# Optimization experiments

Hardware: AMD Instinct MI355X
Metric: run time of the kernel (lower is better)

## Reference

```python
import jax, jax.numpy as jnp
import numpy as np


def _fps(xyz, npoint):
    # Farthest point sampling, vectorized over batch, lax.scan over iterations.
    # Deterministic start at index 0 (torch uses a random start index).
    B, N, _ = xyz.shape
    binds = jnp.arange(B)

    def step(carry, _):
        dist_min, far = carry
        centroid = xyz[binds, far][:, None, :]              # [B,1,3]
        d = jnp.sum((xyz - centroid) ** 2, axis=-1)         # [B,N]
        dist_min = jnp.minimum(dist_min, d)
        return (dist_min, jnp.argmax(dist_min, axis=-1)), far

    init = (jnp.full((B, N), 1e10, xyz.dtype), jnp.zeros((B,), jnp.int32))
    _, cents = jax.lax.scan(step, init, None, length=npoint)
    return cents.T                                           # [B,npoint]


def setup_inputs() -> dict:
    key = jax.random.key(0)
    ks = jax.random.split(key, 8)
    B, N, Cp = 16, 4096, 64
    return {
        "xyz": jax.random.normal(ks[0], (B, N, 3), jnp.float32),
        "points": jax.random.normal(ks[1], (B, Cp, N), jnp.float32),
        "W1": jax.random.normal(ks[2], (64, 67), jnp.float32) * 0.1,
        "b1": jnp.zeros((64,), jnp.float32),
        "W2": jax.random.normal(ks[3], (64, 64), jnp.float32) * 0.1,
        "b2": jnp.zeros((64,), jnp.float32),
        "W3": jax.random.normal(ks[4], (128, 64), jnp.float32) * 0.1,
        "b3": jnp.zeros((128,), jnp.float32),
        "npoint": 1024,
        "k": 32,
    }


def reference(xyz, points, W1, b1, W2, b2, W3, b3, npoint, k):
    B, N, _ = xyz.shape
    binds = jnp.arange(B)

    # FPS -> centroid coords
    cent_idx = _fps(xyz, npoint)                              # [B,S]
    new_xyz = jnp.take_along_axis(xyz, cent_idx[..., None], axis=1)  # [B,S,3]

    # KNN via squared distances (same argsort order as euclidean cdist)
    d2 = (jnp.sum(new_xyz ** 2, -1)[..., None]
          + jnp.sum(xyz ** 2, -1)[:, None, :]
          - 2.0 * jnp.einsum('bsc,bnc->bsn', new_xyz, xyz))   # [B,S,N]
    _, idx = jax.lax.top_k(-d2, k)                            # [B,S,K]

    # Gather-grouping (channels-last; equivalent math to channel-first conv1x1)
    grouped_xyz = xyz[binds[:, None, None], idx]              # [B,S,K,3]
    grouped_pts = points.transpose(0, 2, 1)[binds[:, None, None], idx]  # [B,S,K,Cp]
    grouped = jnp.concatenate([grouped_xyz, grouped_pts], axis=-1)      # [B,S,K,67]

    # Conv2d(k=1) stack == per-point MLP
    h = jax.nn.relu(jnp.einsum('bskc,oc->bsko', grouped, W1) + b1)
    h = jax.nn.relu(jnp.einsum('bskc,oc->bsko', h, W2) + b2)
    h = jax.nn.relu(jnp.einsum('bskc,oc->bsko', h, W3) + b3)  # [B,S,K,128]

    new_points = jnp.max(h, axis=2).transpose(0, 2, 1)        # [B,128,S]
    return new_xyz, new_points
```

## Files before the change

kernel.cpp:

```cpp
#include <hip/hip_runtime.h>
#include <hip/hip_bf16.h>
#include <stdint.h>
#include <string.h>

#define BB   16
#define NN   4096
#define NP   1024
#define KK   32
#define CP   64
#define CIN  67
#define H3   128

typedef __attribute__((ext_vector_type(8))) short short8;
typedef __attribute__((ext_vector_type(4))) float floatx4;
typedef __attribute__((ext_vector_type(2))) float f32x2;

__device__ __forceinline__ float sq3_exact(float x, float y, float z) {
#pragma clang fp contract(off)
    float a = x * x;
    float b = y * y;
    float c = z * z;
    return (a + b) + c;
}
__device__ __forceinline__ float dot3_exact(float ax, float ay, float az,
                                            float bx, float by, float bz) {
#pragma clang fp contract(off)
    float a = ax * bx;
    float b = ay * by;
    float c = az * bz;
    return (a + b) + c;
}
__device__ __forceinline__ float d2_exact(float sn, float sx, float dt) {
#pragma clang fp contract(off)
    return (sn + sx) - 2.0f * dt;
}
__device__ __forceinline__ uint32_t f32_sortable(float f) {
    uint32_t u = __float_as_uint(f);
    return u ^ ((uint32_t)((int32_t)u >> 31) | 0x80000000u);
}
__device__ __forceinline__ unsigned long long umax64(unsigned long long a, unsigned long long b) {
    return a > b ? a : b;
}
__device__ __forceinline__ uint32_t umax32(uint32_t a, uint32_t b) { return a > b ? a : b; }
__device__ __forceinline__ unsigned short bf16_bits(float f) {
    __hip_bfloat16 h = __float2bfloat16(f);
    unsigned short us;
    __builtin_memcpy(&us, &h, 2);
    return us;
}

template <int CTRL>
__device__ __forceinline__ uint32_t dpp_umax32_step(uint32_t k) {
    uint32_t o = (uint32_t)__builtin_amdgcn_update_dpp(0, (int)k, CTRL, 0xf, 0xf, true);
    return k > o ? k : o;
}
__device__ __forceinline__ uint32_t wave_umax32_dpp(uint32_t k) {
    k = dpp_umax32_step<0x111>(k);
    k = dpp_umax32_step<0x112>(k);
    k = dpp_umax32_step<0x114>(k);
    k = dpp_umax32_step<0x118>(k);
    k = dpp_umax32_step<0x142>(k);
    k = dpp_umax32_step<0x143>(k);
    return (uint32_t)__builtin_amdgcn_readlane((int)k, 63);
}

__global__ void __launch_bounds__(256) transpose_pts(const float* __restrict__ pts,
                                                     __hip_bfloat16* __restrict__ ptsT) {
    __shared__ float tile[64][65];
    int b  = blockIdx.y;
    int n0 = blockIdx.x * 64;
    int tx = threadIdx.x & 63, ty = threadIdx.x >> 6;
    const float* src = pts + (size_t)b * CP * NN;
    for (int c = ty; c < 64; c += 4)
        tile[c][tx] = src[c * NN + n0 + tx];
    __syncthreads();
    __hip_bfloat16* dst = ptsT + ((size_t)b * NN + n0) * CP;
    for (int nn2 = ty; nn2 < 64; nn2 += 4)
        dst[nn2 * CP + tx] = __float2bfloat16(tile[tx][nn2]);
}

__global__ void __launch_bounds__(256) prep_weights(const float* __restrict__ W1,
                                                    const float* __restrict__ W2,
                                                    const float* __restrict__ W3,
                                                    short* __restrict__ w1p,
                                                    short* __restrict__ w2p,
                                                    short* __restrict__ w3p) {
    int tid = blockIdx.x * 256 + threadIdx.x;
    int tot = gridDim.x * 256;
    for (int i = tid; i < 64 * 96; i += tot) {
        int o = i / 96, c = i % 96;
        float v = (c < 64) ? W1[o * CIN + 3 + c] : ((c < 67) ? W1[o * CIN + (c - 64)] : 0.0f);
        w1p[i] = (short)bf16_bits(v);
    }
    for (int i = tid; i < 64 * 64; i += tot)  w2p[i] = (short)bf16_bits(W2[i]);
    for (int i = tid; i < 128 * 64; i += tot) w3p[i] = (short)bf16_bits(W3[i]);
}

#define FPS_T 256

__global__ void __launch_bounds__(FPS_T, 1) fps_kernel(const float* __restrict__ xyz,
                                                       float* __restrict__ newxyz) {
    __shared__ __attribute__((aligned(16))) float4 sxyz[NN];
    __shared__ int farr[NP];
    __shared__ __attribute__((aligned(16))) unsigned long long kbuf[2][4];
    int b = blockIdx.x;
    int tid = threadIdx.x;
    const float* xb = xyz + (size_t)b * NN * 3;
    f32x2 px2[8], py2[8], pz2[8], dm2[8];
#pragma unroll
    for (int jj = 0; jj < 8; jj++) {
        int n0 = jj * 512 + tid;
        int n1 = n0 + 256;
        float x0 = xb[n0 * 3 + 0], y0 = xb[n0 * 3 + 1], z0 = xb[n0 * 3 + 2];
        float x1 = xb[n1 * 3 + 0], y1 = xb[n1 * 3 + 1], z1 = xb[n1 * 3 + 2];
        px2[jj] = (f32x2){x0, x1}; py2[jj] = (f32x2){y0, y1}; pz2[jj] = (f32x2){z0, z1};
        sxyz[n0] = make_float4(x0, y0, z0, 0.0f);
        sxyz[n1] = make_float4(x1, y1, z1, 0.0f);
        dm2[jj] = (f32x2){1e10f, 1e10f};
    }
#pragma unroll
    for (int jj = 0; jj < 8; jj++) {
        asm volatile("" : "+v"(px2[jj]), "+v"(py2[jj]), "+v"(pz2[jj]));
    }
    if (tid == 0) farr[0] = 0;
    __syncthreads();
    int far = 0;
    for (int t = 0; t < NP - 1; t++) {
        float4 c = sxyz[far];
        f32x2 ccx = (f32x2){c.x, c.x};
        f32x2 ccy = (f32x2){c.y, c.y};
        f32x2 ccz = (f32x2){c.z, c.z};
        float bv = -1.0f; int bn = 0;
#pragma unroll
        for (int jj = 0; jj < 8; jj++) {
            f32x2 dx, dy, dz, xx, yy, zz, s01, s;
            asm("v_pk_add_f32 %0, %1, %2 neg_lo:[0,1] neg_hi:[0,1]" : "=v"(dx) : "v"(px2[jj]), "v"(ccx));
            asm("v_pk_add_f32 %0, %1, %2 neg_lo:[0,1] neg_hi:[0,1]" : "=v"(dy) : "v"(py2[jj]), "v"(ccy));
            asm("v_pk_add_f32 %0, %1, %2 neg_lo:[0,1] neg_hi:[0,1]" : "=v"(dz) : "v"(pz2[jj]), "v"(ccz));
            asm("v_pk_mul_f32 %0, %1, %1" : "=v"(xx) : "v"(dx));
            asm("v_pk_mul_f32 %0, %1, %1" : "=v"(yy) : "v"(dy));
            asm("v_pk_mul_f32 %0, %1, %1" : "=v"(zz) : "v"(dz));
            asm("v_pk_add_f32 %0, %1, %2" : "=v"(s01) : "v"(xx), "v"(yy));
            asm("v_pk_add_f32 %0, %1, %2" : "=v"(s)   : "v"(s01), "v"(zz));
            float d0 = fminf(dm2[jj].x, s.x);
            dm2[jj].x = d0;
            bn = (d0 > bv) ? (jj * 512 + tid) : bn;
            bv = fmaxf(bv, d0);
            float d1 = fminf(dm2[jj].y, s.y);
            dm2[jj].y = d1;
            bn = (d1 > bv) ? (jj * 512 + 256 + tid) : bn;
            bv = fmaxf(bv, d1);
        }
        uint32_t bvb = __float_as_uint(bv);
        uint32_t m = wave_umax32_dpp(bvb);
        unsigned long long mask = __ballot(bvb == m);
        int n_sel;
        if (__popcll(mask) == 1) {
            n_sel = __builtin_amdgcn_readlane(bn, (int)(__ffsll((unsigned long long)mask) - 1));
        } else {
            uint32_t cand = (bvb == m) ? (uint32_t)bn : 0xFFFFFFFFu;
            n_sel = (int)~wave_umax32_dpp(~cand);
        }
        int par = t & 1;
        if ((tid & 63) == 0)
            kbuf[par][tid >> 6] = ((unsigned long long)m << 32) | (unsigned)(NN - 1 - n_sel);
        __syncthreads();
        const ulonglong2* kp = (const ulonglong2*)kbuf[par];
        ulonglong2 k0 = kp[0], k1 = kp[1];
        unsigned long long mm = umax64(umax64(k0.x, k0.y), umax64(k1.x, k1.y));
        far = NN - 1 - (int)(unsigned)(mm & 0xFFFFFFFFull);
        if (tid == 0) farr[t + 1] = far;
    }
    __syncthreads();
    float* nxb = newxyz + (size_t)b * NP * 3;
    for (int t = tid; t < NP; t += FPS_T) {
        float4 p = sxyz[farr[t]];
        nxb[t * 3 + 0] = p.x;
        nxb[t * 3 + 1] = p.y;
        nxb[t * 3 + 2] = p.z;
    }
}

__global__ void __launch_bounds__(64) knn_kernel(const float* __restrict__ xyz,
                                                 const float* __restrict__ newxyz,
                                                 unsigned short* __restrict__ knn_out) {
    __shared__ uint32_t keys[64 * 64];
    int s = blockIdx.x, b = blockIdx.y, lane = threadIdx.x;
    const float* c3 = newxyz + ((size_t)b * NP + s) * 3;
    float cx = c3[0], cy = c3[1], cz = c3[2];
    float sn = sq3_exact(cx, cy, cz);
    const float* xb = xyz + (size_t)b * NN * 3;
    uint32_t gv[8];
#pragma unroll
    for (int g = 0; g < 8; g++) gv[g] = 0;
#pragma unroll
    for (int j = 0; j < 64; j++) {
        int n = j * 64 + lane;
        float x = xb[n * 3 + 0], y = xb[n * 3 + 1], z = xb[n * 3 + 2];
        float sx = sq3_exact(x, y, z);
        float dt = dot3_exact(cx, cy, cz, x, y, z);
        float d2 = d2_exact(sn, sx, dt);
        uint32_t ck = ~f32_sortable(d2);
        keys[j * 64 + lane] = ck;
        gv[j >> 3] = umax32(gv[j >> 3], ck);
    }
    uint32_t best = 0;
#pragma unroll
    for (int g = 0; g < 8; g++) best = umax32(best, gv[g]);

    unsigned short* out = knn_out + ((size_t)b * NP + s) * KK;
    for (int r = 0; r < KK; r++) {
        uint32_t m = wave_umax32_dpp(best);
        unsigned long long mask = __ballot(best == m);
        bool cand = (best == m);
        uint32_t myn = 0xFFFFFFFFu;
        int gsel = 7, jl = 7;
        uint32_t grp[8];
        if (cand) {
#pragma unroll
            for (int g = 6; g >= 0; g--) if (gv[g] == m) gsel = g;
#pragma unroll
            for (int q = 0; q < 8; q++) grp[q] = keys[(gsel * 8 + q) * 64 + lane];
#pragma unroll
            for (int q = 6; q >= 0; q--) if (grp[q] == m) jl = q;
            myn = (uint32_t)((gsel * 8 + jl) * 64 + lane);
        }
        uint32_t n_sel;
        if (__popcll(mask) > 1) {
            n_sel = ~wave_umax32_dpp(~myn);
        } else {
            n_sel = (uint32_t)__builtin_amdgcn_readlane((int)myn,
                        (int)(__ffsll((unsigned long long)mask) - 1));
        }
        if (lane == 0) out[r] = (unsigned short)n_sel;
        if (cand && myn == n_sel) {
            keys[(gsel * 8 + jl) * 64 + lane] = 0;
#pragma unroll
            for (int q = 0; q < 8; q++) grp[q] = (q == jl) ? 0u : grp[q];
            uint32_t nv = 0;
#pragma unroll
            for (int q = 0; q < 8; q++) nv = umax32(nv, grp[q]);
#pragma unroll
            for (int g = 0; g < 8; g++) gv[g] = (g == gsel) ? nv : gv[g];
            best = 0;
#pragma unroll
            for (int g = 0; g < 8; g++) best = umax32(best, gv[g]);
        }
    }
}

#define MLP_WSZ (32 * 96 + 32 * 72)

__global__ void __launch_bounds__(256) mlp_mfma(const float* __restrict__ xyz,
                                                const __hip_bfloat16* __restrict__ ptsT,
                                                const unsigned short* __restrict__ knni,
                                                const short* __restrict__ w1p,
                                                const short* __restrict__ w2p,
                                                const short* __restrict__ w3p,
                                                const float* __restrict__ b1,
                                                const float* __restrict__ b2,
                                                const float* __restrict__ b3,
                                                float* __restrict__ out_np) {
    __shared__ __attribute__((aligned(16))) short lds[4 * MLP_WSZ];
    int tid  = threadIdx.x;
    int wave = tid >> 6, lane = tid & 63;
    int l15  = lane & 15, quad = lane >> 4;
    int gid  = blockIdx.x * 4 + wave;
    int b    = gid >> 10, s = gid & (NP - 1);
    short* Gw  = lds + wave * MLP_WSZ;
    short* h1w = Gw + 32 * 96;
    short* h2w = Gw;

    float b1v[4], b2v[4], b3v[8];
#pragma unroll
    for (int i = 0; i < 4; i++) b1v[i] = b1[l15 + 16 * i];
#pragma unroll
    for (int i = 0; i < 4; i++) b2v[i] = b2[l15 + 16 * i];
#pragma unroll
    for (int i = 0; i < 8; i++) b3v[i] = b3[l15 + 16 * i];

    {
        int r = lane & 31, h = lane >> 5;
        int n = (int)knni[(size_t)gid * KK + r];
        const short8* prow = (const short8*)(ptsT + ((size_t)b * NN + n) * CP);
        short8 c0 = prow[h * 4 + 0], c1 = prow[h * 4 + 1];
        short8 c2 = prow[h * 4 + 2], c3 = prow[h * 4 + 3];
        short8* gdst = (short8*)&Gw[r * 96];
        gdst[h * 4 + 0] = c0; gdst[h * 4 + 1] = c1;
        gdst[h * 4 + 2] = c2; gdst[h * 4 + 3] = c3;
        short8 z8 = {0, 0, 0, 0, 0, 0, 0, 0};
        if (h == 0) {
            const float* xp = xyz + ((size_t)b * NN + n) * 3;
            short8 v = z8;
            v[0] = (short)bf16_bits(xp[0]);
            v[1] = (short)bf16_bits(xp[1]);
            v[2] = (short)bf16_bits(xp[2]);
            gdst[8] = v; gdst[9] = z8;
        } else {
            gdst[10] = z8; gdst[11] = z8;
        }
    }

    {
        floatx4 acc[2][4];
#pragma unroll
        for (int mt = 0; mt < 2; mt++)
#pragma unroll
            for (int nt = 0; nt < 4; nt++) acc[mt][nt] = (floatx4)0.0f;
#pragma unroll
        for (int kt = 0; kt < 3; kt++) {
            short8 a0 = *(const short8*)&Gw[(l15) * 96 + kt * 32 + quad * 8];
            short8 a1 = *(const short8*)&Gw[(l15 + 16) * 96 + kt * 32 + quad * 8];
#pragma unroll
            for (int nt = 0; nt < 4; nt++) {
                short8 bf = *(const short8*)&w1p[(l15 + 16 * nt) * 96 + kt * 32 + quad * 8];
                acc[0][nt] = __builtin_amdgcn_mfma_f32_16x16x32_bf16(a0, bf, acc[0][nt], 0, 0, 0);
                acc[1][nt] = __builtin_amdgcn_mfma_f32_16x16x32_bf16(a1, bf, acc[1][nt], 0, 0, 0);
            }
        }
#pragma unroll
        for (int mt = 0; mt < 2; mt++)
#pragma unroll
            for (int nt = 0; nt < 4; nt++)
#pragma unroll
                for (int r = 0; r < 4; r++) {
                    float v = fmaxf(acc[mt][nt][r] + b1v[nt], 0.0f);
                    h1w[(quad * 4 + r + 16 * mt) * 72 + l15 + 16 * nt] = (short)bf16_bits(v);
                }
    }

    {
        floatx4 acc[2][4];
#pragma unroll
        for (int mt = 0; mt < 2; mt++)
#pragma unroll
            for (int nt = 0; nt < 4; nt++) acc[mt][nt] = (floatx4)0.0f;
#pragma unroll
        for (int kt = 0; kt < 2; kt++) {
            short8 a0 = *(const short8*)&h1w[(l15) * 72 + kt * 32 + quad * 8];
            short8 a1 = *(const short8*)&h1w[(l15 + 16) * 72 + kt * 32 + quad * 8];
#pragma unroll
            for (int nt = 0; nt < 4; nt++) {
                short8 bf = *(const short8*)&w2p[(l15 + 16 * nt) * 64 + kt * 32 + quad * 8];
                acc[0][nt] = __builtin_amdgcn_mfma_f32_16x16x32_bf16(a0, bf, acc[0][nt], 0, 0, 0);
                acc[1][nt] = __builtin_amdgcn_mfma_f32_16x16x32_bf16(a1, bf, acc[1][nt], 0, 0, 0);
            }
        }
#pragma unroll
        for (int mt = 0; mt < 2; mt++)
#pragma unroll
            for (int nt = 0; nt < 4; nt++)
#pragma unroll
                for (int r = 0; r < 4; r++) {
                    float v = fmaxf(acc[mt][nt][r] + b2v[nt], 0.0f);
                    h2w[(quad * 4 + r + 16 * mt) * 72 + l15 + 16 * nt] = (short)bf16_bits(v);
                }
    }

    {
        floatx4 acc[2][8];
#pragma unroll
        for (int mt = 0; mt < 2; mt++)
#pragma unroll
            for (int nt = 0; nt < 8; nt++) acc[mt][nt] = (floatx4)0.0f;
#pragma unroll
        for (int kt = 0; kt < 2; kt++) {
            short8 a0 = *(const short8*)&h2w[(l15) * 72 + kt * 32 + quad * 8];
            short8 a1 = *(const short8*)&h2w[(l15 + 16) * 72 + kt * 32 + quad * 8];
#pragma unroll
            for (int nt = 0; nt < 8; nt++) {
                short8 bf = *(const short8*)&w3p[(l15 + 16 * nt) * 64 + kt * 32 + quad * 8];
                acc[0][nt] = __builtin_amdgcn_mfma_f32_16x16x32_bf16(a0, bf, acc[0][nt], 0, 0, 0);
                acc[1][nt] = __builtin_amdgcn_mfma_f32_16x16x32_bf16(a1, bf, acc[1][nt], 0, 0, 0);
            }
        }
#pragma unroll
        for (int nt = 0; nt < 8; nt++) {
            float m = acc[0][nt][0];
#pragma unroll
            for (int r = 1; r < 4; r++) m = fmaxf(m, acc[0][nt][r]);
#pragma unroll
            for (int r = 0; r < 4; r++) m = fmaxf(m, acc[1][nt][r]);
            m = fmaxf(m, __shfl_xor(m, 16));
            m = fmaxf(m, __shfl_xor(m, 32));
            m = fmaxf(m + b3v[nt], 0.0f);
            if (lane < 16)
                out_np[((size_t)b * H3 + l15 + 16 * nt) * NP + s] = m;
        }
    }
}

extern "C" void kernel_launch(void* const* d_in, const int* in_sizes, int n_in,
                              void* d_out, int out_size, void* d_ws, size_t ws_size,
                              hipStream_t stream) {
    (void)in_sizes; (void)n_in; (void)out_size; (void)ws_size;
    const float* xyz = (const float*)d_in[0];
    const float* pts = (const float*)d_in[1];
    const float* W1  = (const float*)d_in[2];
    const float* b1  = (const float*)d_in[3];
    const float* W2  = (const float*)d_in[4];
    const float* b2  = (const float*)d_in[5];
    const float* W3  = (const float*)d_in[6];
    const float* b3  = (const float*)d_in[7];

    float* out    = (float*)d_out;
    float* newxyz = out;
    float* newpts = out + (size_t)BB * NP * 3;

    char* ws = (char*)d_ws;
    __hip_bfloat16* ptsT = (__hip_bfloat16*)ws;
    unsigned short* knni = (unsigned short*)(ws + (size_t)BB * NN * CP * 2);
    short* w1p = (short*)(ws + 9437184);
    short* w2p = w1p + 64 * 96;
    short* w3p = w2p + 64 * 64;

    transpose_pts<<<dim3(NN / 64, BB), 256, 0, stream>>>(pts, ptsT);
    prep_weights <<<64, 256, 0, stream>>>(W1, W2, W3, w1p, w2p, w3p);
    fps_kernel   <<<BB, FPS_T, 0, stream>>>(xyz, newxyz);
    knn_kernel   <<<dim3(NP, BB), 64, 0, stream>>>(xyz, newxyz, knni);
    mlp_mfma     <<<dim3(BB * NP / 4), 256, 0, stream>>>(xyz, ptsT, knni,
                                                         w1p, w2p, w3p, b1, b2, b3, newpts);
}
```

Measured before the change: 907.0 us.

## Fuse FPS, KNN and MLP into one persistent kernel with centroid publishing

Replaces the separate FPS, KNN and MLP launches with a single persistent kernel. The first 16 blocks run FPS at raised priority and publish each centroid index to global memory with atomic stores. The remaining worker waves spin on those flags and run KNN plus the MLP per centroid, interleaved across batches. This overlaps the serial FPS latency with the KNN/MLP work and removes the KNN index round-trip through global memory. The cost is spin-wait polling, and correctness depends on the FPS blocks being co-resident with the workers so the spinning cannot deadlock.

Result: faster. 762.2 us (-16.0%).

```diff
diff --git a/kernel.cpp b/kernel.cpp
--- a/kernel.cpp
+++ b/kernel.cpp
@@ -10,6 +10,11 @@
 #define CP   64
 #define CIN  67
 #define H3   128
+
+#define FPS_T   256
+#define NWORKB  496
+#define NGRID   (BB + NWORKB)
+#define NWAVES  (NWORKB * 4)
 
 typedef __attribute__((ext_vector_type(8))) short short8;
 typedef __attribute__((ext_vector_type(4))) float floatx4;
@@ -84,9 +89,11 @@
                                                     const float* __restrict__ W3,
                                                     short* __restrict__ w1p,
                                                     short* __restrict__ w2p,
-                                                    short* __restrict__ w3p) {
+                                                    short* __restrict__ w3p,
+                                                    uint32_t* __restrict__ centpub) {
     int tid = blockIdx.x * 256 + threadIdx.x;
     int tot = gridDim.x * 256;
+    for (int i = tid; i < BB * NP; i += tot) centpub[i] = 0u;
     for (int i = tid; i < 64 * 96; i += tot) {
         int o = i / 96, c = i % 96;
         float v = (c < 64) ? W1[o * CIN + 3 + c] : ((c < 67) ? W1[o * CIN + (c - 64)] : 0.0f);
@@ -96,180 +103,118 @@
     for (int i = tid; i < 128 * 64; i += tot) w3p[i] = (short)bf16_bits(W3[i]);
 }
 
-#define FPS_T 256
-
-__global__ void __launch_bounds__(FPS_T, 1) fps_kernel(const float* __restrict__ xyz,
-                                                       float* __restrict__ newxyz) {
-    __shared__ __attribute__((aligned(16))) float4 sxyz[NN];
-    __shared__ int farr[NP];
-    __shared__ __attribute__((aligned(16))) unsigned long long kbuf[2][4];
-    int b = blockIdx.x;
+__global__ void __launch_bounds__(256, 2)
+fused_kernel(const float* __restrict__ xyz,
+             const __hip_bfloat16* __restrict__ ptsT,
+             const short* __restrict__ w1p,
+             const short* __restrict__ w2p,
+             const short* __restrict__ w3p,
+             const float* __restrict__ b1,
+             const float* __restrict__ b2,
+             const float* __restrict__ b3,
+             uint32_t* __restrict__ centpub,
+             float* __restrict__ out) {
+    __shared__ __attribute__((aligned(16))) char smem[69696];
     int tid = threadIdx.x;
-    const float* xb = xyz + (size_t)b * NN * 3;
-    f32x2 px2[8], py2[8], pz2[8], dm2[8];
-#pragma unroll
-    for (int jj = 0; jj < 8; jj++) {
-        int n0 = jj * 512 + tid;
-        int n1 = n0 + 256;
-        float x0 = xb[n0 * 3 + 0], y0 = xb[n0 * 3 + 1], z0 = xb[n0 * 3 + 2];
-        float x1 = xb[n1 * 3 + 0], y1 = xb[n1 * 3 + 1], z1 = xb[n1 * 3 + 2];
-        px2[jj] = (f32x2){x0, x1}; py2[jj] = (f32x2){y0, y1}; pz2[jj] = (f32x2){z0, z1};
-        sxyz[n0] = make_float4(x0, y0, z0, 0.0f);
-        sxyz[n1] = make_float4(x1, y1, z1, 0.0f);
-        dm2[jj] = (f32x2){1e10f, 1e10f};
+
+    if (blockIdx.x < BB) {
+        asm volatile("s_setprio 3");
+        float4* sxyz = (float4*)smem;
+        int*    farr = (int*)(smem + 65536);
+        unsigned long long* kbufp = (unsigned long long*)(smem + 69632);
+        int b = blockIdx.x;
+        uint32_t* pub = centpub + b * NP;
+        const float* xb = xyz + (size_t)b * NN * 3;
+        if (tid == 0)
+            __hip_atomic_store(&pub[0], 0x10000u, __ATOMIC_RELAXED, __HIP_MEMORY_SCOPE_AGENT);
+        f32x2 px2[8], py2[8], pz2[8], dm2[8];
+#pragma unroll
+        for (int jj = 0; jj < 8; jj++) {
+            int n0 = jj * 512 + tid;
+            int n1 = n0 + 256;
+            float x0 = xb[n0 * 3 + 0], y0 = xb[n0 * 3 + 1], z0 = xb[n0 * 3 + 2];
+            float x1 = xb[n1 * 3 + 0], y1 = xb[n1 * 3 + 1], z1 = xb[n1 * 3 + 2];
+            px2[jj] = (f32x2){x0, x1}; py2[jj] = (f32x2){y0, y1}; pz2[jj] = (f32x2){z0, z1};
+            sxyz[n0] = make_float4(x0, y0, z0, 0.0f);
+            sxyz[n1] = make_float4(x1, y1, z1, 0.0f);
+            dm2[jj] = (f32x2){1e10f, 1e10f};
+        }
+#pragma unroll
+        for (int jj = 0; jj < 8; jj++) {
+            asm volatile("" : "+v"(px2[jj]), "+v"(py2[jj]), "+v"(pz2[jj]));
+        }
+        if (tid == 0) farr[0] = 0;
+        __syncthreads();
+        int far = 0;
+        for (int t = 0; t < NP - 1; t++) {
+            float4 c = sxyz[far];
+            f32x2 ccx = (f32x2){c.x, c.x};
+            f32x2 ccy = (f32x2){c.y, c.y};
+            f32x2 ccz = (f32x2){c.z, c.z};
+            float bv = -1.0f; int bn = 0;
+#pragma unroll
+            for (int jj = 0; jj < 8; jj++) {
+                f32x2 dx, dy, dz, xx, yy, zz, s01, s;
+                asm("v_pk_add_f32 %0, %1, %2 neg_lo:[0,1] neg_hi:[0,1]" : "=v"(dx) : "v"(px2[jj]), "v"(ccx));
+                asm("v_pk_add_f32 %0, %1, %2 neg_lo:[0,1] neg_hi:[0,1]" : "=v"(dy) : "v"(py2[jj]), "v"(ccy));
+                asm("v_pk_add_f32 %0, %1, %2 neg_lo:[0,1] neg_hi:[0,1]" : "=v"(dz) : "v"(pz2[jj]), "v"(ccz));
+                asm("v_pk_mul_f32 %0, %1, %1" : "=v"(xx) : "v"(dx));
+                asm("v_pk_mul_f32 %0, %1, %1" : "=v"(yy) : "v"(dy));
+                asm("v_pk_mul_f32 %0, %1, %1" : "=v"(zz) : "v"(dz));
+                asm("v_pk_add_f32 %0, %1, %2" : "=v"(s01) : "v"(xx), "v"(yy));
+                asm("v_pk_add_f32 %0, %1, %2" : "=v"(s)   : "v"(s01), "v"(zz));
+                float d0 = fminf(dm2[jj].x, s.x);
+                dm2[jj].x = d0;
+                bn = (d0 > bv) ? (jj * 512 + tid) : bn;
+                bv = fmaxf(bv, d0);
+                float d1 = fminf(dm2[jj].y, s.y);
+                dm2[jj].y = d1;
+                bn = (d1 > bv) ? (jj * 512 + 256 + tid) : bn;
+                bv = fmaxf(bv, d1);
+            }
+            uint32_t bvb = __float_as_uint(bv);
+            uint32_t m = wave_umax32_dpp(bvb);
+            unsigned long long mask = __ballot(bvb == m);
+            int n_sel;
+            if (__popcll(mask) == 1) {
+                n_sel = __builtin_amdgcn_readlane(bn, (int)(__ffsll((unsigned long long)mask) - 1));
+            } else {
+                uint32_t cand = (bvb == m) ? (uint32_t)bn : 0xFFFFFFFFu;
+                n_sel = (int)~wave_umax32_dpp(~cand);
+            }
+            int par = t & 1;
+            if ((tid & 63) == 0)
+                kbufp[par * 4 + (tid >> 6)] =
+                    ((unsigned long long)m << 32) | (unsigned)(NN - 1 - n_sel);
+            __syncthreads();
+            const ulonglong2* kp = (const ulonglong2*)(kbufp + par * 4);
+            ulonglong2 k0 = kp[0], k1 = kp[1];
+            unsigned long long mm = umax64(umax64(k0.x, k0.y), umax64(k1.x, k1.y));
+            far = NN - 1 - (int)(unsigned)(mm & 0xFFFFFFFFull);
+            if (tid == 0) {
+                farr[t + 1] = far;
+                __hip_atomic_store(&pub[t + 1], 0x10000u | (uint32_t)far,
+                                   __ATOMIC_RELAXED, __HIP_MEMORY_SCOPE_AGENT);
+            }
+        }
+        __syncthreads();
+        float* nxb = out + (size_t)b * NP * 3;
+        for (int t = tid; t < NP; t += FPS_T) {
+            float4 p = sxyz[farr[t]];
+            nxb[t * 3 + 0] = p.x;
+            nxb[t * 3 + 1] = p.y;
+            nxb[t * 3 + 2] = p.z;
+        }
+        return;
     }
-#pragma unroll
-    for (int jj = 0; jj < 8; jj++) {
-        asm volatile("" : "+v"(px2[jj]), "+v"(py2[jj]), "+v"(pz2[jj]));
-    }
-    if (tid == 0) farr[0] = 0;
-    __syncthreads();
-    int far = 0;
-    for (int t = 0; t < NP - 1; t++) {
-        float4 c = sxyz[far];
-        f32x2 ccx = (f32x2){c.x, c.x};
-        f32x2 ccy = (f32x2){c.y, c.y};
-        f32x2 ccz = (f32x2){c.z, c.z};
-        float bv = -1.0f; int bn = 0;
-#pragma unroll
-        for (int jj = 0; jj < 8; jj++) {
-            f32x2 dx, dy, dz, xx, yy, zz, s01, s;
-            asm("v_pk_add_f32 %0, %1, %2 neg_lo:[0,1] neg_hi:[0,1]" : "=v"(dx) : "v"(px2[jj]), "v"(ccx));
-            asm("v_pk_add_f32 %0, %1, %2 neg_lo:[0,1] neg_hi:[0,1]" : "=v"(dy) : "v"(py2[jj]), "v"(ccy));
-            asm("v_pk_add_f32 %0, %1, %2 neg_lo:[0,1] neg_hi:[0,1]" : "=v"(dz) : "v"(pz2[jj]), "v"(ccz));
-            asm("v_pk_mul_f32 %0, %1, %1" : "=v"(xx) : "v"(dx));
-            asm("v_pk_mul_f32 %0, %1, %1" : "=v"(yy) : "v"(dy));
-            asm("v_pk_mul_f32 %0, %1, %1" : "=v"(zz) : "v"(dz));
-            asm("v_pk_add_f32 %0, %1, %2" : "=v"(s01) : "v"(xx), "v"(yy));
-            asm("v_pk_add_f32 %0, %1, %2" : "=v"(s)   : "v"(s01), "v"(zz));
-            float d0 = fminf(dm2[jj].x, s.x);
-            dm2[jj].x = d0;
-            bn = (d0 > bv) ? (jj * 512 + tid) : bn;
-            bv = fmaxf(bv, d0);
-            float d1 = fminf(dm2[jj].y, s.y);
-            dm2[jj].y = d1;
-            bn = (d1 > bv) ? (jj * 512 + 256 + tid) : bn;
-            bv = fmaxf(bv, d1);
-        }
-        uint32_t bvb = __float_as_uint(bv);
-        uint32_t m = wave_umax32_dpp(bvb);
-        unsigned long long mask = __ballot(bvb == m);
-        int n_sel;
-        if (__popcll(mask) == 1) {
-            n_sel = __builtin_amdgcn_readlane(bn, (int)(__ffsll((unsigned long long)mask) - 1));
-        } else {
-            uint32_t cand = (bvb == m) ? (uint32_t)bn : 0xFFFFFFFFu;
-            n_sel = (int)~wave_umax32_dpp(~cand);
-        }
-        int par = t & 1;
-        if ((tid & 63) == 0)
-            kbuf[par][tid >> 6] = ((unsigned long long)m << 32) | (unsigned)(NN - 1 - n_sel);
-        __syncthreads();
-        const ulonglong2* kp = (const ulonglong2*)kbuf[par];
-        ulonglong2 k0 = kp[0], k1 = kp[1];
-        unsigned long long mm = umax64(umax64(k0.x, k0.y), umax64(k1.x, k1.y));
-        far = NN - 1 - (int)(unsigned)(mm & 0xFFFFFFFFull);
-        if (tid == 0) farr[t + 1] = far;
-    }
-    __syncthreads();
-    float* nxb = newxyz + (size_t)b * NP * 3;
-    for (int t = tid; t < NP; t += FPS_T) {
-        float4 p = sxyz[farr[t]];
-        nxb[t * 3 + 0] = p.x;
-        nxb[t * 3 + 1] = p.y;
-        nxb[t * 3 + 2] = p.z;
-    }
-}
-
-__global__ void __launch_bounds__(64) knn_kernel(const float* __restrict__ xyz,
-                                                 const float* __restrict__ newxyz,
-                                                 unsigned short* __restrict__ knn_out) {
-    __shared__ uint32_t keys[64 * 64];
-    int s = blockIdx.x, b = blockIdx.y, lane = threadIdx.x;
-    const float* c3 = newxyz + ((size_t)b * NP + s) * 3;
-    float cx = c3[0], cy = c3[1], cz = c3[2];
-    float sn = sq3_exact(cx, cy, cz);
-    const float* xb = xyz + (size_t)b * NN * 3;
-    uint32_t gv[8];
-#pragma unroll
-    for (int g = 0; g < 8; g++) gv[g] = 0;
-#pragma unroll
-    for (int j = 0; j < 64; j++) {
-        int n = j * 64 + lane;
-        float x = xb[n * 3 + 0], y = xb[n * 3 + 1], z = xb[n * 3 + 2];
-        float sx = sq3_exact(x, y, z);
-        float dt = dot3_exact(cx, cy, cz, x, y, z);
-        float d2 = d2_exact(sn, sx, dt);
-        uint32_t ck = ~f32_sortable(d2);
-        keys[j * 64 + lane] = ck;
-        gv[j >> 3] = umax32(gv[j >> 3], ck);
-    }
-    uint32_t best = 0;
-#pragma unroll
-    for (int g = 0; g < 8; g++) best = umax32(best, gv[g]);
-
-    unsigned short* out = knn_out + ((size_t)b * NP + s) * KK;
-    for (int r = 0; r < KK; r++) {
-        uint32_t m = wave_umax32_dpp(best);
-        unsigned long long mask = __ballot(best == m);
-        bool cand = (best == m);
-        uint32_t myn = 0xFFFFFFFFu;
-        int gsel = 7, jl = 7;
-        uint32_t grp[8];
-        if (cand) {
-#pragma unroll
-            for (int g = 6; g >= 0; g--) if (gv[g] == m) gsel = g;
-#pragma unroll
-            for (int q = 0; q < 8; q++) grp[q] = keys[(gsel * 8 + q) * 64 + lane];
-#pragma unroll
-            for (int q = 6; q >= 0; q--) if (grp[q] == m) jl = q;
-            myn = (uint32_t)((gsel * 8 + jl) * 64 + lane);
-        }
-        uint32_t n_sel;
-        if (__popcll(mask) > 1) {
-            n_sel = ~wave_umax32_dpp(~myn);
-        } else {
-            n_sel = (uint32_t)__builtin_amdgcn_readlane((int)myn,
-                        (int)(__ffsll((unsigned long long)mask) - 1));
-        }
-        if (lane == 0) out[r] = (unsigned short)n_sel;
-        if (cand && myn == n_sel) {
-            keys[(gsel * 8 + jl) * 64 + lane] = 0;
-#pragma unroll
-            for (int q = 0; q < 8; q++) grp[q] = (q == jl) ? 0u : grp[q];
-            uint32_t nv = 0;
-#pragma unroll
-            for (int q = 0; q < 8; q++) nv = umax32(nv, grp[q]);
-#pragma unroll
-            for (int g = 0; g < 8; g++) gv[g] = (g == gsel) ? nv : gv[g];
-            best = 0;
-#pragma unroll
-            for (int g = 0; g < 8; g++) best = umax32(best, gv[g]);
-        }
-    }
-}
-
-#define MLP_WSZ (32 * 96 + 32 * 72)
-
-__global__ void __launch_bounds__(256) mlp_mfma(const float* __restrict__ xyz,
-                                                const __hip_bfloat16* __restrict__ ptsT,
-                                                const unsigned short* __restrict__ knni,
-                                                const short* __restrict__ w1p,
-                                                const short* __restrict__ w2p,
-                                                const short* __restrict__ w3p,
-                                                const float* __restrict__ b1,
-                                                const float* __restrict__ b2,
-                                                const float* __restrict__ b3,
-                                                float* __restrict__ out_np) {
-    __shared__ __attribute__((aligned(16))) short lds[4 * MLP_WSZ];
-    int tid  = threadIdx.x;
+
     int wave = tid >> 6, lane = tid & 63;
     int l15  = lane & 15, quad = lane >> 4;
-    int gid  = blockIdx.x * 4 + wave;
-    int b    = gid >> 10, s = gid & (NP - 1);
-    short* Gw  = lds + wave * MLP_WSZ;
-    short* h1w = Gw + 32 * 96;
-    short* h2w = Gw;
+    int wv   = (blockIdx.x - BB) * 4 + wave;
+    uint32_t* keys = (uint32_t*)smem + wave * NN;
+    short* mG  = (short*)keys;
+    short* mh1 = mG + 32 * 96;
+    float* out_np = out + (size_t)BB * NP * 3;
 
     float b1v[4], b2v[4], b3v[8];
 #pragma unroll
@@ -279,113 +224,186 @@
 #pragma unroll
     for (int i = 0; i < 8; i++) b3v[i] = b3[l15 + 16 * i];
 
-    {
-        int r = lane & 31, h = lane >> 5;
-        int n = (int)knni[(size_t)gid * KK + r];
-        const short8* prow = (const short8*)(ptsT + ((size_t)b * NN + n) * CP);
-        short8 c0 = prow[h * 4 + 0], c1 = prow[h * 4 + 1];
-        short8 c2 = prow[h * 4 + 2], c3 = prow[h * 4 + 3];
-        short8* gdst = (short8*)&Gw[r * 96];
-        gdst[h * 4 + 0] = c0; gdst[h * 4 + 1] = c1;
-        gdst[h * 4 + 2] = c2; gdst[h * 4 + 3] = c3;
-        short8 z8 = {0, 0, 0, 0, 0, 0, 0, 0};
-        if (h == 0) {
-            const float* xp = xyz + ((size_t)b * NN + n) * 3;
-            short8 v = z8;
-            v[0] = (short)bf16_bits(xp[0]);
-            v[1] = (short)bf16_bits(xp[1]);
-            v[2] = (short)bf16_bits(xp[2]);
-            gdst[8] = v; gdst[9] = z8;
-        } else {
-            gdst[10] = z8; gdst[11] = z8;
-        }
-    }
-
-    {
-        floatx4 acc[2][4];
-#pragma unroll
-        for (int mt = 0; mt < 2; mt++)
-#pragma unroll
-            for (int nt = 0; nt < 4; nt++) acc[mt][nt] = (floatx4)0.0f;
-#pragma unroll
-        for (int kt = 0; kt < 3; kt++) {
-            short8 a0 = *(const short8*)&Gw[(l15) * 96 + kt * 32 + quad * 8];
-            short8 a1 = *(const short8*)&Gw[(l15 + 16) * 96 + kt * 32 + quad * 8];
-#pragma unroll
-            for (int nt = 0; nt < 4; nt++) {
-                short8 bf = *(const short8*)&w1p[(l15 + 16 * nt) * 96 + kt * 32 + quad * 8];
-                acc[0][nt] = __builtin_amdgcn_mfma_f32_16x16x32_bf16(a0, bf, acc[0][nt], 0, 0, 0);
-                acc[1][nt] = __builtin_amdgcn_mfma_f32_16x16x32_bf16(a1, bf, acc[1][nt], 0, 0, 0);
-            }
-        }
-#pragma unroll
-        for (int mt = 0; mt < 2; mt++)
-#pragma unroll
-            for (int nt = 0; nt < 4; nt++)
-#pragma unroll
-                for (int r = 0; r < 4; r++) {
-                    float v = fmaxf(acc[mt][nt][r] + b1v[nt], 0.0f);
-                    h1w[(quad * 4 + r + 16 * mt) * 72 + l15 + 16 * nt] = (short)bf16_bits(v);
+    for (int task = wv; task < BB * NP; task += NWAVES) {
+        int s = task >> 4, b = task & (BB - 1);
+        const float* xb = xyz + (size_t)b * NN * 3;
+        uint32_t v;
+        for (;;) {
+            v = __hip_atomic_load(&centpub[b * NP + s], __ATOMIC_RELAXED,
+                                  __HIP_MEMORY_SCOPE_AGENT);
+            if ((v >> 16) == 1u) break;
+            __builtin_amdgcn_s_sleep(2);
+        }
+        int fr = (int)(v & 0xFFFFu);
+        float cx = xb[fr * 3 + 0], cy = xb[fr * 3 + 1], cz = xb[fr * 3 + 2];
+        float sn = sq3_exact(cx, cy, cz);
+
+        asm volatile("" ::: "memory");
+        uint32_t gv[8];
+#pragma unroll
+        for (int g = 0; g < 8; g++) gv[g] = 0;
+#pragma unroll
+        for (int j = 0; j < 64; j++) {
+            int n = j * 64 + lane;
+            float x = xb[n * 3 + 0], y = xb[n * 3 + 1], z = xb[n * 3 + 2];
+            float sx = sq3_exact(x, y, z);
+            float dt = dot3_exact(cx, cy, cz, x, y, z);
+            float d2 = d2_exact(sn, sx, dt);
+            uint32_t ck = ~f32_sortable(d2);
+            keys[j * 64 + lane] = ck;
+            gv[j >> 3] = umax32(gv[j >> 3], ck);
+        }
+        uint32_t best = 0;
+#pragma unroll
+        for (int g = 0; g < 8; g++) best = umax32(best, gv[g]);
+
+        uint32_t myidx = 0;
+        for (int r = 0; r < KK; r++) {
+            uint32_t m = wave_umax32_dpp(best);
+            unsigned long long mask = __ballot(best == m);
+            bool cand = (best == m);
+            uint32_t myn = 0xFFFFFFFFu;
+            int gsel = 7, jl = 7;
+            uint32_t grp[8];
+            if (cand) {
+#pragma unroll
+                for (int g = 6; g >= 0; g--) if (gv[g] == m) gsel = g;
+#pragma unroll
+                for (int q = 0; q < 8; q++) grp[q] = keys[(gsel * 8 + q) * 64 + lane];
+#pragma unroll
+                for (int q = 6; q >= 0; q--) if (grp[q] == m) jl = q;
+                myn = (uint32_t)((gsel * 8 + jl) * 64 + lane);
+            }
+            uint32_t n_sel;
+            if (__popcll(mask) > 1) {
+                n_sel = ~wave_umax32_dpp(~myn);
+            } else {
+                n_sel = (uint32_t)__builtin_amdgcn_readlane((int)myn,
+                            (int)(__ffsll((unsigned long long)mask) - 1));
+            }
+            if (lane == r) myidx = n_sel;
+            if (cand && myn == n_sel) {
+                keys[(gsel * 8 + jl) * 64 + lane] = 0;
+#pragma unroll
+                for (int q = 0; q < 8; q++) grp[q] = (q == jl) ? 0u : grp[q];
+                uint32_t nv = 0;
+#pragma unroll
+                for (int q = 0; q < 8; q++) nv = umax32(nv, grp[q]);
+#pragma unroll
+                for (int g = 0; g < 8; g++) gv[g] = (g == gsel) ? nv : gv[g];
+                best = 0;
+#pragma unroll
+                for (int g = 0; g < 8; g++) best = umax32(best, gv[g]);
+            }
+        }
+        asm volatile("" ::: "memory");
+
+        {
+            int rr = lane & 31, h = lane >> 5;
+            int n = __shfl((int)myidx, rr);
+            const short8* prow = (const short8*)(ptsT + ((size_t)b * NN + n) * CP);
+            short8 c0 = prow[h * 4 + 0], c1 = prow[h * 4 + 1];
+            short8 c2 = prow[h * 4 + 2], c3 = prow[h * 4 + 3];
+            short8* gdst = (short8*)&mG[rr * 96];
+            gdst[h * 4 + 0] = c0; gdst[h * 4 + 1] = c1;
+            gdst[h * 4 + 2] = c2; gdst[h * 4 + 3] = c3;
+            short8 z8 = {0, 0, 0, 0, 0, 0, 0, 0};
+            if (h == 0) {
+                const float* xp = xyz + ((size_t)b * NN + n) * 3;
+                short8 vx = z8;
+                vx[0] = (short)bf16_bits(xp[0]);
+                vx[1] = (short)bf16_bits(xp[1]);
+                vx[2] = (short)bf16_bits(xp[2]);
+                gdst[8] = vx; gdst[9] = z8;
+            } else {
+                gdst[10] = z8; gdst[11] = z8;
+            }
+        }
+        {
+            floatx4 acc[2][4];
+#pragma unroll
+            for (int mt = 0; mt < 2; mt++)
+#pragma unroll
+                for (int nt = 0; nt < 4; nt++) acc[mt][nt] = (floatx4)0.0f;
+#pragma unroll
+            for (int kt = 0; kt < 3; kt++) {
+                short8 a0 = *(const short8*)&mG[(l15) * 96 + kt * 32 + quad * 8];
+                short8 a1 = *(const short8*)&mG[(l15 + 16) * 96 + kt * 32 + quad * 8];
+#pragma unroll
+                for (int nt = 0; nt < 4; nt++) {
+                    short8 bf = *(const short8*)&w1p[(l15 + 16 * nt) * 96 + kt * 32 + quad * 8];
+                    acc[0][nt] = __builtin_amdgcn_mfma_f32_16x16x32_bf16(a0, bf, acc[0][nt], 0, 0, 0);
+                    acc[1][nt] = __builtin_amdgcn_mfma_f32_16x16x32_bf16(a1, bf, acc[1][nt], 0, 0, 0);
                 }
-    }
-
-    {
-        floatx4 acc[2][4];
-#pragma unroll
-        for (int mt = 0; mt < 2; mt++)
-#pragma unroll
-            for (int nt = 0; nt < 4; nt++) acc[mt][nt] = (floatx4)0.0f;
-#pragma unroll
-        for (int kt = 0; kt < 2; kt++) {
-            short8 a0 = *(const short8*)&h1w[(l15) * 72 + kt * 32 + quad * 8];
-            short8 a1 = *(const short8*)&h1w[(l15 + 16) * 72 + kt * 32 + quad * 8];
-#pragma unroll
-            for (int nt = 0; nt < 4; nt++) {
-                short8 bf = *(const short8*)&w2p[(l15 + 16 * nt) * 64 + kt * 32 + quad * 8];
-                acc[0][nt] = __builtin_amdgcn_mfma_f32_16x16x32_bf16(a0, bf, acc[0][nt], 0, 0, 0);
-                acc[1][nt] = __builtin_amdgcn_mfma_f32_16x16x32_bf16(a1, bf, acc[1][nt], 0, 0, 0);
-            }
-        }
-#pragma unroll
-        for (int mt = 0; mt < 2; mt++)
-#pragma unroll
-            for (int nt = 0; nt < 4; nt++)
-#pragma unroll
-                for (int r = 0; r < 4; r++) {
-                    float v = fmaxf(acc[mt][nt][r] + b2v[nt], 0.0f);
-                    h2w[(quad * 4 + r + 16 * mt) * 72 + l15 + 16 * nt] = (short)bf16_bits(v);
+            }
+#pragma unroll
+            for (int mt = 0; mt < 2; mt++)
+#pragma unroll
+                for (int nt = 0; nt < 4; nt++)
+#pragma unroll
+                    for (int r = 0; r < 4; r++) {
+                        float vv = fmaxf(acc[mt][nt][r] + b1v[nt], 0.0f);
+                        mh1[(quad * 4 + r + 16 * mt) * 72 + l15 + 16 * nt] = (short)bf16_bits(vv);
+                    }
+        }
+        asm volatile("" ::: "memory");
+        {
+            floatx4 acc[2][4];
+#pragma unroll
+            for (int mt = 0; mt < 2; mt++)
+#pragma unroll
+                for (int nt = 0; nt < 4; nt++) acc[mt][nt] = (floatx4)0.0f;
+#pragma unroll
+            for (int kt = 0; kt < 2; kt++) {
+                short8 a0 = *(const short8*)&mh1[(l15) * 72 + kt * 32 + quad * 8];
+                short8 a1 = *(const short8*)&mh1[(l15 + 16) * 72 + kt * 32 + quad * 8];
+#pragma unroll
+                for (int nt = 0; nt < 4; nt++) {
+                    short8 bf = *(const short8*)&w2p[(l15 + 16 * nt) * 64 + kt * 32 + quad * 8];
+                    acc[0][nt] = __builtin_amdgcn_mfma_f32_16x16x32_bf16(a0, bf, acc[0][nt], 0, 0, 0);
+                    acc[1][nt] = __builtin_amdgcn_mfma_f32_16x16x32_bf16(a1, bf, acc[1][nt], 0, 0, 0);
                 }
-    }
-
-    {
-        floatx4 acc[2][8];
-#pragma unroll
-        for (int mt = 0; mt < 2; mt++)
-#pragma unroll
-            for (int nt = 0; nt < 8; nt++) acc[mt][nt] = (floatx4)0.0f;
-#pragma unroll
-        for (int kt = 0; kt < 2; kt++) {
-            short8 a0 = *(const short8*)&h2w[(l15) * 72 + kt * 32 + quad * 8];
-            short8 a1 = *(const short8*)&h2w[(l15 + 16) * 72 + kt * 32 + quad * 8];
+            }
+#pragma unroll
+            for (int mt = 0; mt < 2; mt++)
+#pragma unroll
+                for (int nt = 0; nt < 4; nt++)
+#pragma unroll
+                    for (int r = 0; r < 4; r++) {
+                        float vv = fmaxf(acc[mt][nt][r] + b2v[nt], 0.0f);
+                        mG[(quad * 4 + r + 16 * mt) * 72 + l15 + 16 * nt] = (short)bf16_bits(vv);
+                    }
+        }
+        {
+            floatx4 acc[2][8];
+#pragma unroll
+            for (int mt = 0; mt < 2; mt++)
+#pragma unroll
+                for (int nt = 0; nt < 8; nt++) acc[mt][nt] = (floatx4)0.0f;
+#pragma unroll
+            for (int kt = 0; kt < 2; kt++) {
+                short8 a0 = *(const short8*)&mG[(l15) * 72 + kt * 32 + quad * 8];
+                short8 a1 = *(const short8*)&mG[(l15 + 16) * 72 + kt * 32 + quad * 8];
+#pragma unroll
+                for (int nt = 0; nt < 8; nt++) {
+                    short8 bf = *(const short8*)&w3p[(l15 + 16 * nt) * 64 + kt * 32 + quad * 8];
+                    acc[0][nt] = __builtin_amdgcn_mfma_f32_16x16x32_bf16(a0, bf, acc[0][nt], 0, 0, 0);
+                    acc[1][nt] = __builtin_amdgcn_mfma_f32_16x16x32_bf16(a1, bf, acc[1][nt], 0, 0, 0);
+                }
+            }
 #pragma unroll
             for (int nt = 0; nt < 8; nt++) {
-                short8 bf = *(const short8*)&w3p[(l15 + 16 * nt) * 64 + kt * 32 + quad * 8];
-                acc[0][nt] = __builtin_amdgcn_mfma_f32_16x16x32_bf16(a0, bf, acc[0][nt], 0, 0, 0);
-                acc[1][nt] = __builtin_amdgcn_mfma_f32_16x16x32_bf16(a1, bf, acc[1][nt], 0, 0, 0);
-            }
-        }
-#pragma unroll
-        for (int nt = 0; nt < 8; nt++) {
-            float m = acc[0][nt][0];
-#pragma unroll
-            for (int r = 1; r < 4; r++) m = fmaxf(m, acc[0][nt][r]);
-#pragma unroll
-            for (int r = 0; r < 4; r++) m = fmaxf(m, acc[1][nt][r]);
-            m = fmaxf(m, __shfl_xor(m, 16));
-            m = fmaxf(m, __shfl_xor(m, 32));
-            m = fmaxf(m + b3v[nt], 0.0f);
-            if (lane < 16)
-                out_np[((size_t)b * H3 + l15 + 16 * nt) * NP + s] = m;
+                float m = acc[0][nt][0];
+#pragma unroll
+                for (int r = 1; r < 4; r++) m = fmaxf(m, acc[0][nt][r]);
+#pragma unroll
+                for (int r = 0; r < 4; r++) m = fmaxf(m, acc[1][nt][r]);
+                m = fmaxf(m, __shfl_xor(m, 16));
+                m = fmaxf(m, __shfl_xor(m, 32));
+                m = fmaxf(m + b3v[nt], 0.0f);
+                if (lane < 16)
+                    out_np[((size_t)b * H3 + l15 + 16 * nt) * NP + s] = m;
+            }
         }
     }
 }
@@ -403,21 +421,17 @@
     const float* W3  = (const float*)d_in[6];
     const float* b3  = (const float*)d_in[7];
 
-    float* out    = (float*)d_out;
-    float* newxyz = out;
-    float* newpts = out + (size_t)BB * NP * 3;
+    float* out = (float*)d_out;
 
     char* ws = (char*)d_ws;
     __hip_bfloat16* ptsT = (__hip_bfloat16*)ws;
-    unsigned short* knni = (unsigned short*)(ws + (size_t)BB * NN * CP * 2);
+    uint32_t* centpub = (uint32_t*)(ws + 8388608);
     short* w1p = (short*)(ws + 9437184);
     short* w2p = w1p + 64 * 96;
     short* w3p = w2p + 64 * 64;
 
     transpose_pts<<<dim3(NN / 64, BB), 256, 0, stream>>>(pts, ptsT);
-    prep_weights <<<64, 256, 0, stream>>>(W1, W2, W3, w1p, w2p, w3p);
-    fps_kernel   <<<BB, FPS_T, 0, stream>>>(xyz, newxyz);
-    knn_kernel   <<<dim3(NP, BB), 64, 0, stream>>>(xyz, newxyz, knni);
-    mlp_mfma     <<<dim3(BB * NP / 4), 256, 0, stream>>>(xyz, ptsT, knni,
-                                                         w1p, w2p, w3p, b1, b2, b3, newpts);
-}
+    prep_weights <<<64, 256, 0, stream>>>(W1, W2, W3, w1p, w2p, w3p, centpub);
+    fused_kernel <<<NGRID, 256, 0, stream>>>(xyz, ptsT, w1p, w2p, w3p,
+                                             b1, b2, b3, centpub, out);
+}
```
